# Kernel optimization log

Hardware: AMD Instinct MI355X
Metric: run time of the kernel (lower is better)

The kernel has to match this reference:

```python
import jax, jax.numpy as jnp
import numpy as np

D_MODEL = 1024
N_HEAD = 16
HEAD_DIM = D_MODEL // N_HEAD


def setup_inputs() -> dict:
    key = jax.random.key(0)
    ks = jax.random.split(key, 5)
    s_attn = 1.0 / np.sqrt(D_MODEL)
    s_proj = 1.0 / np.sqrt(D_MODEL)
    return {
        "x": jax.random.normal(ks[0], (4, 2048, D_MODEL), dtype=jnp.float32),
        "w_attn": jax.random.normal(ks[1], (D_MODEL, 3 * D_MODEL), dtype=jnp.float32) * s_attn,
        "b_attn": jax.random.normal(ks[2], (3 * D_MODEL,), dtype=jnp.float32) * 0.02,
        "w_proj": jax.random.normal(ks[3], (D_MODEL, D_MODEL), dtype=jnp.float32) * s_proj,
        "b_proj": jax.random.normal(ks[4], (D_MODEL,), dtype=jnp.float32) * 0.02,
    }


def reference(x, w_attn, b_attn, w_proj, b_proj):
    B, T, C = x.shape
    qkv = x @ w_attn + b_attn  # [B,T,3C]
    q, k, v = jnp.split(qkv, 3, axis=2)
    # [B,T,C] -> [B,H,T,Dh]
    def heads(t):
        return t.reshape(B, T, N_HEAD, HEAD_DIM).transpose(0, 2, 1, 3)
    q, k, v = heads(q), heads(k), heads(v)
    scale = 1.0 / np.sqrt(HEAD_DIM)
    att = jnp.einsum("bhqd,bhkd->bhqk", q, k) * scale
    att = jax.nn.softmax(att, axis=-1)  # NOTE: no causal mask in source
    y = jnp.einsum("bhqk,bhkd->bhqd", att, v)
    y = y.transpose(0, 2, 1, 3).reshape(B, T, C)
    return y @ w_proj + b_proj
```

## Files before the change

kernel.cpp:

```cpp
#include <hip/hip_runtime.h>
#include <hip/hip_bf16.h>
#include <cstdint>
#include <cstddef>

#define DI __device__ __forceinline__

typedef float f32x4 __attribute__((ext_vector_type(4)));
typedef short short8 __attribute__((ext_vector_type(8)));
typedef unsigned short us4 __attribute__((ext_vector_type(4)));
typedef unsigned int u32x2 __attribute__((ext_vector_type(2)));

constexpr int Bc = 4, Tc = 2048, Cc = 1024, Hc = 16, Dhc = 64;
constexpr int Mrows = Bc * Tc;
constexpr int N1 = 3 * Cc;
constexpr int K1 = Cc;

DI unsigned short f2bf(float f) {
  unsigned u = __builtin_bit_cast(unsigned, f);
  unsigned r = u + 0x7FFFu + ((u >> 16) & 1u);
  return (unsigned short)(r >> 16);
}
DI float bf2f(unsigned short h) {
  return __builtin_bit_cast(float, (unsigned)h << 16);
}
DI unsigned cvtpk(float a, float b) {
  unsigned r;
  asm("v_cvt_pk_bf16_f32 %0, %1, %2" : "=v"(r) : "v"(a), "v"(b));
  return r;
}

#define GLOAD16(gp, lp)                                                        \
  __builtin_amdgcn_global_load_lds(                                            \
      (const __attribute__((address_space(1))) void*)(gp),                     \
      (__attribute__((address_space(3))) void*)(lp), 16, 0, 0)

__global__ __launch_bounds__(256) void k_cast_x(const float* __restrict__ x,
                                                unsigned short* __restrict__ xb) {
  int i = (blockIdx.x * 256 + threadIdx.x) * 8;
  f32x4 a = *reinterpret_cast<const f32x4*>(x + i);
  f32x4 b = *reinterpret_cast<const f32x4*>(x + i + 4);
  us4 r0 = {f2bf(a[0]), f2bf(a[1]), f2bf(a[2]), f2bf(a[3])};
  us4 r1 = {f2bf(b[0]), f2bf(b[1]), f2bf(b[2]), f2bf(b[3])};
  *reinterpret_cast<us4*>(xb + i) = r0;
  *reinterpret_cast<us4*>(xb + i + 4) = r1;
}

__global__ __launch_bounds__(256) void k_transpose_bf(const float* __restrict__ w,
                                                      unsigned short* __restrict__ wT,
                                                      int Kd, int Nd) {
  __shared__ float t[64][65];
  int kb = blockIdx.y * 64, nb = blockIdx.x * 64;
  int c = threadIdx.x & 63, r4 = threadIdx.x >> 6;
#pragma unroll
  for (int it = 0; it < 16; ++it) {
    int r = it * 4 + r4;
    t[r][c] = w[(size_t)(kb + r) * Nd + nb + c];
  }
  __syncthreads();
#pragma unroll
  for (int it = 0; it < 16; ++it) {
    int r = it * 4 + r4;
    wT[(size_t)(nb + r) * Kd + kb + c] = f2bf(t[c][r]);
  }
}

__global__ __launch_bounds__(256) void k_transpose_split(const float* __restrict__ w,
                                                         unsigned short* __restrict__ whi,
                                                         unsigned short* __restrict__ wlo) {
  __shared__ float t[64][65];
  int kb = blockIdx.y * 64, nb = blockIdx.x * 64;
  int c = threadIdx.x & 63, r4 = threadIdx.x >> 6;
#pragma unroll
  for (int it = 0; it < 16; ++it) {
    int r = it * 4 + r4;
    t[r][c] = w[(size_t)(kb + r) * Cc + nb + c];
  }
  __syncthreads();
#pragma unroll
  for (int it = 0; it < 16; ++it) {
    int r = it * 4 + r4;
    float v = t[c][r];
    unsigned short hi = f2bf(v);
    float rem = v - bf2f(hi);
    size_t idx = (size_t)(nb + r) * Cc + kb + c;
    whi[idx] = hi;
    wlo[idx] = f2bf(rem);
  }
}

__global__ __launch_bounds__(256) void k_gemm_qkv(
    const unsigned short* __restrict__ xb, const unsigned short* __restrict__ waT,
    const float* __restrict__ bias, unsigned short* __restrict__ q,
    unsigned short* __restrict__ kkp, unsigned short* __restrict__ vT) {
  __shared__ unsigned short lA[128 * 64];
  __shared__ unsigned short lB[128 * 64];
  const int tid = threadIdx.x, lane = tid & 63, wid = tid >> 6;
  const int wr = wid >> 1, wc = wid & 1;
  const int l15 = lane & 15, l4 = lane >> 4;
  const int rowBase = blockIdx.y * 128;
  const int colBase = blockIdx.x * 128;

  f32x4 acc[4][4] = {};

  for (int kt = 0; kt < K1 / 64; ++kt) {
    __syncthreads();
#pragma unroll
    for (int ch = 0; ch < 4; ++ch) {
      int d = wid * 4096 + ch * 1024 + lane * 16;
      int r = d >> 7;
      int cbyte = (d & 127) ^ ((r & 7) << 4);
      const unsigned short* ga = xb + (size_t)(rowBase + r) * K1 + kt * 64 + (cbyte >> 1);
      GLOAD16(ga, (char*)lA + wid * 4096 + ch * 1024);
      const unsigned short* gb = waT + (size_t)(colBase + r) * K1 + kt * 64 + (cbyte >> 1);
      GLOAD16(gb, (char*)lB + wid * 4096 + ch * 1024);
    }
    __syncthreads();
#pragma unroll
    for (int ks = 0; ks < 2; ++ks) {
      short8 af[4], bfv[4];
#pragma unroll
      for (int mf = 0; mf < 4; ++mf) {
        int r = wr * 64 + mf * 16 + l15;
        af[mf] = *reinterpret_cast<const short8*>(
            (const char*)lA + r * 128 + ((ks * 64 + (l4 << 4)) ^ ((r & 7) << 4)));
      }
#pragma unroll
      for (int nf = 0; nf < 4; ++nf) {
        int r = wc * 64 + nf * 16 + l15;
        bfv[nf] = *reinterpret_cast<const short8*>(
            (const char*)lB + r * 128 + ((ks * 64 + (l4 << 4)) ^ ((r & 7) << 4)));
      }
#pragma unroll
      for (int mf = 0; mf < 4; ++mf)
#pragma unroll
        for (int nf = 0; nf < 4; ++nf)
          acc[mf][nf] = __builtin_amdgcn_mfma_f32_16x16x32_bf16(af[mf], bfv[nf],
                                                                acc[mf][nf], 0, 0, 0);
    }
  }
  const int sec = colBase >> 10;
#pragma unroll
  for (int nf = 0; nf < 4; ++nf) {
    int ccol = colBase + wc * 64 + nf * 16 + l15;
    float bv = bias[ccol];
    int cc = ccol & 1023;
    int h = cc >> 6, dd = cc & 63;
#pragma unroll
    for (int mf = 0; mf < 4; ++mf) {
      int r0 = rowBase + wr * 64 + mf * 16 + l4 * 4;
      f32x4 v = acc[mf][nf];
      if (sec == 2) {
        int b_ = r0 >> 11, t = r0 & 2047;
        int pair = b_ * 16 + h;
        us4 pk = {f2bf(v[0] + bv), f2bf(v[1] + bv), f2bf(v[2] + bv), f2bf(v[3] + bv)};
        *reinterpret_cast<us4*>(vT + ((size_t)pair * 64 + dd) * 2048 + t) = pk;
      } else {
        unsigned short* dst = (sec == 0) ? q : kkp;
#pragma unroll
        for (int j = 0; j < 4; ++j) {
          int r = r0 + j;
          int b_ = r >> 11, t = r & 2047;
          dst[((size_t)(b_ * 16 + h) * 2048 + t) * 64 + dd] = f2bf(v[j] + bv);
        }
      }
    }
  }
}

__global__ __launch_bounds__(512) void k_attn(
    const unsigned short* __restrict__ q, const unsigned short* __restrict__ kkp,
    const unsigned short* __restrict__ vT, unsigned short* __restrict__ yh,
    unsigned short* __restrict__ yl) {
  __shared__ unsigned short lK[2][64 * 64];
  __shared__ unsigned short lV[2][64 * 64];
  __shared__ unsigned short lP[8][32 * 64];
  const int tid = threadIdx.x, lane = tid & 63, wid = tid >> 6;
  const int l15 = lane & 15, l4 = lane >> 4;
  const int qb = blockIdx.x, pair = blockIdx.y;
  const size_t base = (size_t)pair * Tc * Dhc;
  const int swz = (l15 & 7) << 4;

  const int sd = wid * 1024 + lane * 16;
  const int sr = sd >> 7;
  const int scb = (sd & 127) ^ ((sr & 7) << 4);
  const unsigned short* gkbase = kkp + base + (size_t)sr * 64 + (scb >> 1);
  const unsigned short* gvbase = vT + base + (size_t)sr * 2048 + (scb >> 1);

  short8 qf[2][2];
#pragma unroll
  for (int qt = 0; qt < 2; ++qt) {
    int qrow = qb * 256 + wid * 32 + qt * 16 + l15;
#pragma unroll
    for (int ks = 0; ks < 2; ++ks)
      qf[qt][ks] = *reinterpret_cast<const short8*>(q + base + (size_t)qrow * 64 +
                                                    ks * 32 + l4 * 8);
  }

  f32x4 yac[2][4] = {};
  float lsum[2] = {0.f, 0.f};
  constexpr float C1 = 0.18033688011112042f;
  char* lPw = (char*)lP[wid];

  GLOAD16(gkbase, (char*)lK[0] + wid * 1024);
  GLOAD16(gvbase, (char*)lV[0] + wid * 1024);

  for (int kb = 0; kb < Tc / 64; ++kb) {
    const int b = kb & 1;
    asm volatile("s_waitcnt vmcnt(0)" ::: "memory");
    __builtin_amdgcn_s_barrier();
    if (kb < Tc / 64 - 1) {
      GLOAD16(gkbase + (size_t)(kb + 1) * 4096, (char*)lK[b ^ 1] + wid * 1024);
      GLOAD16(gvbase + (kb + 1) * 64, (char*)lV[b ^ 1] + wid * 1024);
    }

    const char* lKb = (const char*)lK[b];
#pragma unroll
    for (int nf = 0; nf < 4; ++nf) {
      int r = nf * 16 + l15;
      f32x4 s0 = {0.f, 0.f, 0.f, 0.f}, s1 = {0.f, 0.f, 0.f, 0.f};
      __builtin_amdgcn_s_setprio(1);
#pragma unroll
      for (int ks = 0; ks < 2; ++ks) {
        short8 kf = *reinterpret_cast<const short8*>(
            lKb + r * 128 + ((ks * 64 + (l4 << 4)) ^ swz));
        s0 = __builtin_amdgcn_mfma_f32_16x16x32_bf16(kf, qf[0][ks], s0, 0, 0, 0);
        s1 = __builtin_amdgcn_mfma_f32_16x16x32_bf16(kf, qf[1][ks], s1, 0, 0, 0);
      }
      __builtin_amdgcn_s_setprio(0);
      float p0 = __builtin_amdgcn_exp2f(s0[0] * C1);
      float p1 = __builtin_amdgcn_exp2f(s0[1] * C1);
      float p2 = __builtin_amdgcn_exp2f(s0[2] * C1);
      float p3 = __builtin_amdgcn_exp2f(s0[3] * C1);
      lsum[0] += (p0 + p1) + (p2 + p3);
      u32x2 w0 = {cvtpk(p0, p1), cvtpk(p2, p3)};
      *reinterpret_cast<u32x2*>(lPw + l15 * 128 + ((nf * 32 + l4 * 8) ^ swz)) = w0;
      p0 = __builtin_amdgcn_exp2f(s1[0] * C1);
      p1 = __builtin_amdgcn_exp2f(s1[1] * C1);
      p2 = __builtin_amdgcn_exp2f(s1[2] * C1);
      p3 = __builtin_amdgcn_exp2f(s1[3] * C1);
      lsum[1] += (p0 + p1) + (p2 + p3);
      u32x2 w1 = {cvtpk(p0, p1), cvtpk(p2, p3)};
      *reinterpret_cast<u32x2*>(lPw + (16 + l15) * 128 + ((nf * 32 + l4 * 8) ^ swz)) = w1;
    }
    const char* lVb = (const char*)lV[b];
    __builtin_amdgcn_s_setprio(1);
#pragma unroll
    for (int ks = 0; ks < 2; ++ks) {
      short8 pf0 = *reinterpret_cast<const short8*>(
          lPw + l15 * 128 + ((ks * 64 + (l4 << 4)) ^ swz));
      short8 pf1 = *reinterpret_cast<const short8*>(
          lPw + (16 + l15) * 128 + ((ks * 64 + (l4 << 4)) ^ swz));
#pragma unroll
      for (int mf = 0; mf < 4; ++mf) {
        int r = mf * 16 + l15;
        short8 vf = *reinterpret_cast<const short8*>(
            lVb + r * 128 + ((ks * 64 + (l4 << 4)) ^ swz));
        yac[0][mf] = __builtin_amdgcn_mfma_f32_16x16x32_bf16(vf, pf0, yac[0][mf], 0, 0, 0);
        yac[1][mf] = __builtin_amdgcn_mfma_f32_16x16x32_bf16(vf, pf1, yac[1][mf], 0, 0, 0);
      }
    }
    __builtin_amdgcn_s_setprio(0);
  }
  const int b_ = pair >> 4, h = pair & 15;
#pragma unroll
  for (int qt = 0; qt < 2; ++qt) {
    float l = lsum[qt];
    l += __shfl_xor(l, 16);
    l += __shfl_xor(l, 32);
    float invl = 1.0f / l;
    size_t rowg = (size_t)(b_ * 2048 + qb * 256 + wid * 32 + qt * 16 + l15);
#pragma unroll
    for (int mf = 0; mf < 4; ++mf) {
      f32x4 v = yac[qt][mf];
      us4 hi, lo;
#pragma unroll
      for (int j = 0; j < 4; ++j) {
        float f = v[j] * invl;
        unsigned short h1 = f2bf(f);
        hi[j] = h1;
        lo[j] = f2bf(f - bf2f(h1));
      }
      size_t off = rowg * 1024 + h * 64 + mf * 16 + l4 * 4;
      *reinterpret_cast<us4*>(yh + off) = hi;
      *reinterpret_cast<us4*>(yl + off) = lo;
    }
  }
}

__global__ __launch_bounds__(256) void k_gemm_proj(
    const unsigned short* __restrict__ yh, const unsigned short* __restrict__ yl,
    const unsigned short* __restrict__ wph, const unsigned short* __restrict__ wpl,
    const float* __restrict__ bias, float* __restrict__ out) {
  __shared__ unsigned short lAh[64 * 64], lAl[64 * 64];
  __shared__ unsigned short lBh[128 * 64], lBl[128 * 64];
  const int tid = threadIdx.x, lane = tid & 63, wid = tid >> 6;
  const int wr = wid >> 1, wc = wid & 1;
  const int l15 = lane & 15, l4 = lane >> 4;
  const int rowBase = blockIdx.y * 64;
  const int colBase = blockIdx.x * 128;

  f32x4 acc[2][4] = {};

  for (int kt = 0; kt < 16; ++kt) {
    __syncthreads();
#pragma unroll
    for (int ch = 0; ch < 2; ++ch) {
      int d = wid * 2048 + ch * 1024 + lane * 16;
      int r = d >> 7;
      int cbyte = (d & 127) ^ ((r & 7) << 4);
      const unsigned short* gah = yh + (size_t)(rowBase + r) * Cc + kt * 64 + (cbyte >> 1);
      GLOAD16(gah, (char*)lAh + wid * 2048 + ch * 1024);
      const unsigned short* gal = yl + (size_t)(rowBase + r) * Cc + kt * 64 + (cbyte >> 1);
      GLOAD16(gal, (char*)lAl + wid * 2048 + ch * 1024);
    }
#pragma unroll
    for (int ch = 0; ch < 4; ++ch) {
      int d = wid * 4096 + ch * 1024 + lane * 16;
      int r = d >> 7;
      int cbyte = (d & 127) ^ ((r & 7) << 4);
      const unsigned short* gbh = wph + (size_t)(colBase + r) * Cc + kt * 64 + (cbyte >> 1);
      GLOAD16(gbh, (char*)lBh + wid * 4096 + ch * 1024);
      const unsigned short* gbl = wpl + (size_t)(colBase + r) * Cc + kt * 64 + (cbyte >> 1);
      GLOAD16(gbl, (char*)lBl + wid * 4096 + ch * 1024);
    }
    __syncthreads();
#pragma unroll
    for (int ks = 0; ks < 2; ++ks) {
      short8 ah[2], al_[2], bh[4], bl[4];
#pragma unroll
      for (int mf = 0; mf < 2; ++mf) {
        int r = wr * 32 + mf * 16 + l15;
        int off = r * 128 + ((ks * 64 + (l4 << 4)) ^ ((r & 7) << 4));
        ah[mf] = *reinterpret_cast<const short8*>((const char*)lAh + off);
        al_[mf] = *reinterpret_cast<const short8*>((const char*)lAl + off);
      }
#pragma unroll
      for (int nf = 0; nf < 4; ++nf) {
        int r = wc * 64 + nf * 16 + l15;
        int off = r * 128 + ((ks * 64 + (l4 << 4)) ^ ((r & 7) << 4));
        bh[nf] = *reinterpret_cast<const short8*>((const char*)lBh + off);
        bl[nf] = *reinterpret_cast<const short8*>((const char*)lBl + off);
      }
#pragma unroll
      for (int mf = 0; mf < 2; ++mf)
#pragma unroll
        for (int nf = 0; nf < 4; ++nf) {
          acc[mf][nf] = __builtin_amdgcn_mfma_f32_16x16x32_bf16(ah[mf], bh[nf],
                                                                acc[mf][nf], 0, 0, 0);
          acc[mf][nf] = __builtin_amdgcn_mfma_f32_16x16x32_bf16(ah[mf], bl[nf],
                                                                acc[mf][nf], 0, 0, 0);
          acc[mf][nf] = __builtin_amdgcn_mfma_f32_16x16x32_bf16(al_[mf], bh[nf],
                                                                acc[mf][nf], 0, 0, 0);
        }
    }
  }
#pragma unroll
  for (int nf = 0; nf < 4; ++nf) {
    int c = colBase + wc * 64 + nf * 16 + l15;
    float bv = bias[c];
#pragma unroll
    for (int mf = 0; mf < 2; ++mf) {
      int r0 = rowBase + wr * 32 + mf * 16 + l4 * 4;
      f32x4 v = acc[mf][nf];
#pragma unroll
      for (int j = 0; j < 4; ++j) out[(size_t)(r0 + j) * Cc + c] = v[j] + bv;
    }
  }
}

extern "C" void kernel_launch(void* const* d_in, const int* in_sizes, int n_in,
                              void* d_out, int out_size, void* d_ws, size_t ws_size,
                              hipStream_t stream) {
  const float* x = (const float*)d_in[0];
  const float* w_attn = (const float*)d_in[1];
  const float* b_attn = (const float*)d_in[2];
  const float* w_proj = (const float*)d_in[3];
  const float* b_proj = (const float*)d_in[4];
  float* out = (float*)d_out;
  char* ws = (char*)d_ws;
  const size_t MiB = 1u << 20;
  unsigned short* xb = (unsigned short*)(ws + 0 * MiB);
  unsigned short* waT = (unsigned short*)(ws + 16 * MiB);
  unsigned short* q = (unsigned short*)(ws + 22 * MiB);
  unsigned short* kk = (unsigned short*)(ws + 38 * MiB);
  unsigned short* vT = (unsigned short*)(ws + 54 * MiB);
  unsigned short* yh = (unsigned short*)(ws + 70 * MiB);
  unsigned short* yl = (unsigned short*)(ws + 86 * MiB);
  unsigned short* wph = (unsigned short*)(ws + 102 * MiB);
  unsigned short* wpl = (unsigned short*)(ws + 104 * MiB);

  k_cast_x<<<dim3(4096), dim3(256), 0, stream>>>(x, xb);
  k_transpose_bf<<<dim3(48, 16), dim3(256), 0, stream>>>(w_attn, waT, K1, N1);
  k_transpose_split<<<dim3(16, 16), dim3(256), 0, stream>>>(w_proj, wph, wpl);
  k_gemm_qkv<<<dim3(24, 64), dim3(256), 0, stream>>>(xb, waT, b_attn, q, kk, vT);
  k_attn<<<dim3(8, 64), dim3(512), 0, stream>>>(q, kk, vT, yh, yl);
  k_gemm_proj<<<dim3(8, 128), dim3(256), 0, stream>>>(yh, yl, wph, wpl, b_proj, out);
}
```

Measured before the change: 310.2 us.

## Fold softmax scale into Q epilogue and restructure proj GEMM as 3-pass K loop

Multiplies the Q section of the QKV GEMM epilogue by the log2-domain softmax scale, so the attention inner loop drops a multiply per score before exp2. The split-precision projection GEMM is rewritten to use 128x128 tiles, treating the hi/lo products as a concatenated K of 48 steps over single A/B LDS buffers rather than loading four buffers and issuing three MFMAs per step. This cuts per-step LDS traffic and raises reuse per block, at the cost of fewer blocks (512) and Q being rounded to bf16 after scaling, which slightly changes numerics.

```diff
diff --git a/kernel.cpp b/kernel.cpp
--- a/kernel.cpp
+++ b/kernel.cpp
@@ -138,7 +138,9 @@
                                                                 acc[mf][nf], 0, 0, 0);
     }
   }
+  constexpr float C1 = 0.18033688011112042f;
   const int sec = colBase >> 10;
+  const float qsc = (sec == 0) ? C1 : 1.0f;
 #pragma unroll
   for (int nf = 0; nf < 4; ++nf) {
     int ccol = colBase + wc * 64 + nf * 16 + l15;
@@ -160,7 +162,7 @@
         for (int j = 0; j < 4; ++j) {
           int r = r0 + j;
           int b_ = r >> 11, t = r & 2047;
-          dst[((size_t)(b_ * 16 + h) * 2048 + t) * 64 + dd] = f2bf(v[j] + bv);
+          dst[((size_t)(b_ * 16 + h) * 2048 + t) * 64 + dd] = f2bf((v[j] + bv) * qsc);
         }
       }
     }
@@ -198,7 +200,6 @@
 
   f32x4 yac[2][4] = {};
   float lsum[2] = {0.f, 0.f};
-  constexpr float C1 = 0.18033688011112042f;
   char* lPw = (char*)lP[wid];
 
   GLOAD16(gkbase, (char*)lK[0] + wid * 1024);
@@ -227,17 +228,17 @@
         s1 = __builtin_amdgcn_mfma_f32_16x16x32_bf16(kf, qf[1][ks], s1, 0, 0, 0);
       }
       __builtin_amdgcn_s_setprio(0);
-      float p0 = __builtin_amdgcn_exp2f(s0[0] * C1);
-      float p1 = __builtin_amdgcn_exp2f(s0[1] * C1);
-      float p2 = __builtin_amdgcn_exp2f(s0[2] * C1);
-      float p3 = __builtin_amdgcn_exp2f(s0[3] * C1);
+      float p0 = __builtin_amdgcn_exp2f(s0[0]);
+      float p1 = __builtin_amdgcn_exp2f(s0[1]);
+      float p2 = __builtin_amdgcn_exp2f(s0[2]);
+      float p3 = __builtin_amdgcn_exp2f(s0[3]);
       lsum[0] += (p0 + p1) + (p2 + p3);
       u32x2 w0 = {cvtpk(p0, p1), cvtpk(p2, p3)};
       *reinterpret_cast<u32x2*>(lPw + l15 * 128 + ((nf * 32 + l4 * 8) ^ swz)) = w0;
-      p0 = __builtin_amdgcn_exp2f(s1[0] * C1);
-      p1 = __builtin_amdgcn_exp2f(s1[1] * C1);
-      p2 = __builtin_amdgcn_exp2f(s1[2] * C1);
-      p3 = __builtin_amdgcn_exp2f(s1[3] * C1);
+      p0 = __builtin_amdgcn_exp2f(s1[0]);
+      p1 = __builtin_amdgcn_exp2f(s1[1]);
+      p2 = __builtin_amdgcn_exp2f(s1[2]);
+      p3 = __builtin_amdgcn_exp2f(s1[3]);
       lsum[1] += (p0 + p1) + (p2 + p3);
       u32x2 w1 = {cvtpk(p0, p1), cvtpk(p2, p3)};
       *reinterpret_cast<u32x2*>(lPw + (16 + l15) * 128 + ((nf * 32 + l4 * 8) ^ swz)) = w1;
@@ -291,67 +292,53 @@
     const unsigned short* __restrict__ yh, const unsigned short* __restrict__ yl,
     const unsigned short* __restrict__ wph, const unsigned short* __restrict__ wpl,
     const float* __restrict__ bias, float* __restrict__ out) {
-  __shared__ unsigned short lAh[64 * 64], lAl[64 * 64];
-  __shared__ unsigned short lBh[128 * 64], lBl[128 * 64];
+  __shared__ unsigned short lA[128 * 64];
+  __shared__ unsigned short lB[128 * 64];
   const int tid = threadIdx.x, lane = tid & 63, wid = tid >> 6;
   const int wr = wid >> 1, wc = wid & 1;
   const int l15 = lane & 15, l4 = lane >> 4;
-  const int rowBase = blockIdx.y * 64;
+  const int rowBase = blockIdx.y * 128;
   const int colBase = blockIdx.x * 128;
 
-  f32x4 acc[2][4] = {};
-
-  for (int kt = 0; kt < 16; ++kt) {
+  f32x4 acc[4][4] = {};
+
+  for (int kt = 0; kt < 48; ++kt) {
+    const unsigned short* As = (kt < 32) ? yh : yl;
+    const unsigned short* Bs = (kt < 16) ? wph : (kt < 32 ? wpl : wph);
+    const int kOff = (kt & 15) * 64;
     __syncthreads();
-#pragma unroll
-    for (int ch = 0; ch < 2; ++ch) {
-      int d = wid * 2048 + ch * 1024 + lane * 16;
-      int r = d >> 7;
-      int cbyte = (d & 127) ^ ((r & 7) << 4);
-      const unsigned short* gah = yh + (size_t)(rowBase + r) * Cc + kt * 64 + (cbyte >> 1);
-      GLOAD16(gah, (char*)lAh + wid * 2048 + ch * 1024);
-      const unsigned short* gal = yl + (size_t)(rowBase + r) * Cc + kt * 64 + (cbyte >> 1);
-      GLOAD16(gal, (char*)lAl + wid * 2048 + ch * 1024);
-    }
 #pragma unroll
     for (int ch = 0; ch < 4; ++ch) {
       int d = wid * 4096 + ch * 1024 + lane * 16;
       int r = d >> 7;
       int cbyte = (d & 127) ^ ((r & 7) << 4);
-      const unsigned short* gbh = wph + (size_t)(colBase + r) * Cc + kt * 64 + (cbyte >> 1);
-      GLOAD16(gbh, (char*)lBh + wid * 4096 + ch * 1024);
-      const unsigned short* gbl = wpl + (size_t)(colBase + r) * Cc + kt * 64 + (cbyte >> 1);
-      GLOAD16(gbl, (char*)lBl + wid * 4096 + ch * 1024);
+      const unsigned short* ga = As + (size_t)(rowBase + r) * Cc + kOff + (cbyte >> 1);
+      GLOAD16(ga, (char*)lA + wid * 4096 + ch * 1024);
+      const unsigned short* gb = Bs + (size_t)(colBase + r) * Cc + kOff + (cbyte >> 1);
+      GLOAD16(gb, (char*)lB + wid * 4096 + ch * 1024);
     }
     __syncthreads();
 #pragma unroll
     for (int ks = 0; ks < 2; ++ks) {
-      short8 ah[2], al_[2], bh[4], bl[4];
-#pragma unroll
-      for (int mf = 0; mf < 2; ++mf) {
-        int r = wr * 32 + mf * 16 + l15;
-        int off = r * 128 + ((ks * 64 + (l4 << 4)) ^ ((r & 7) << 4));
-        ah[mf] = *reinterpret_cast<const short8*>((const char*)lAh + off);
-        al_[mf] = *reinterpret_cast<const short8*>((const char*)lAl + off);
+      short8 af[4], bfv[4];
+#pragma unroll
+      for (int mf = 0; mf < 4; ++mf) {
+        int r = wr * 64 + mf * 16 + l15;
+        af[mf] = *reinterpret_cast<const short8*>(
+            (const char*)lA + r * 128 + ((ks * 64 + (l4 << 4)) ^ ((r & 7) << 4)));
       }
 #pragma unroll
       for (int nf = 0; nf < 4; ++nf) {
         int r = wc * 64 + nf * 16 + l15;
-        int off = r * 128 + ((ks * 64 + (l4 << 4)) ^ ((r & 7) << 4));
-        bh[nf] = *reinterpret_cast<const short8*>((const char*)lBh + off);
-        bl[nf] = *reinterpret_cast<const short8*>((const char*)lBl + off);
-      }
-#pragma unroll
-      for (int mf = 0; mf < 2; ++mf)
-#pragma unroll
-        for (int nf = 0; nf < 4; ++nf) {
-          acc[mf][nf] = __builtin_amdgcn_mfma_f32_16x16x32_bf16(ah[mf], bh[nf],
+        bfv[nf] = *reinterpret_cast<const short8*>(
+            (const char*)lB + r * 128 + ((ks * 64 + (l4 << 4)) ^ ((r & 7) << 4)));
+      }
+#pragma unroll
+      for (int mf = 0; mf < 4; ++mf)
+#pragma unroll
+        for (int nf = 0; nf < 4; ++nf)
+          acc[mf][nf] = __builtin_amdgcn_mfma_f32_16x16x32_bf16(af[mf], bfv[nf],
                                                                 acc[mf][nf], 0, 0, 0);
-          acc[mf][nf] = __builtin_amdgcn_mfma_f32_16x16x32_bf16(ah[mf], bl[nf],
-                                                                acc[mf][nf], 0, 0, 0);
-          acc[mf][nf] = __builtin_amdgcn_mfma_f32_16x16x32_bf16(al_[mf], bh[nf],
-                                                                acc[mf][nf], 0, 0, 0);
-        }
     }
   }
 #pragma unroll
@@ -359,8 +346,8 @@
     int c = colBase + wc * 64 + nf * 16 + l15;
     float bv = bias[c];
 #pragma unroll
-    for (int mf = 0; mf < 2; ++mf) {
-      int r0 = rowBase + wr * 32 + mf * 16 + l4 * 4;
+    for (int mf = 0; mf < 4; ++mf) {
+      int r0 = rowBase + wr * 64 + mf * 16 + l4 * 4;
       f32x4 v = acc[mf][nf];
 #pragma unroll
       for (int j = 0; j < 4; ++j) out[(size_t)(r0 + j) * Cc + c] = v[j] + bv;
@@ -394,5 +381,5 @@
   k_transpose_split<<<dim3(16, 16), dim3(256), 0, stream>>>(w_proj, wph, wpl);
   k_gemm_qkv<<<dim3(24, 64), dim3(256), 0, stream>>>(xb, waT, b_attn, q, kk, vT);
   k_attn<<<dim3(8, 64), dim3(512), 0, stream>>>(q, kk, vT, yh, yl);
-  k_gemm_proj<<<dim3(8, 128), dim3(256), 0, stream>>>(yh, yl, wph, wpl, b_proj, out);
-}
+  k_gemm_proj<<<dim3(8, 64), dim3(256), 0, stream>>>(yh, yl, wph, wpl, b_proj, out);
+}
```

New measurement: 317.0 us. 2.2% more time.
